# Optimization experiments

Measured on AMD Instinct MI355X. Metric: run time of the kernel, lower is better.

Reference implementation:

```python
import jax, jax.numpy as jnp
import numpy as np

MAX_DISP = 4
RANGE = 2 * MAX_DISP + 1  # 9 -> 80 output channels (center skipped)


def setup_inputs() -> dict:
    key = jax.random.key(0)
    k1, k2 = jax.random.split(key)
    B, C, H, W = 8, 128, 160, 160
    feat1 = jax.random.normal(k1, (B, C, H, W), dtype=jnp.float32)
    feat2 = jax.random.normal(k2, (B, C, H, W), dtype=jnp.float32)
    return {"feat1": feat1, "feat2": feat2}


def cost_volume(feat1, feat2):
    B, C, H, W = feat1.shape
    pad = MAX_DISP
    # zero-pad feat2 spatially by max_displacement on all sides
    feat2_padded = jnp.pad(feat2, ((0, 0), (0, 0), (pad, pad), (pad, pad)))
    vols = []
    for i in range(RANGE):
        for j in range(RANGE):
            if i == pad and j == pad:
                continue  # original skips the zero-displacement center
            feat2_slice = feat2_padded[:, :, i:i + H, j:j + W]  # [B,C,H,W]
            # channel-mean of elementwise product -> [B,1,H,W]
            corr = jnp.mean(feat1 * feat2_slice, axis=1, keepdims=True)
            vols.append(corr)
    return jnp.concatenate(vols, axis=1)  # [B, 80, H, W]


def reference(feat1, feat2):
    return cost_volume(feat1, feat2)
```

## Files before the change

kernel.cpp:

```cpp
#include <hip/hip_runtime.h>

#define BB 8
#define CC_ALL 128
#define HH 160
#define WW 160
#define PAD 4
#define RANGE 9
#define ND 80
#define NG 3
#define DR 3
#define TH 8
#define NTX 40
#define PXT 4
#define NTHREADS 960
#define CCHUNK 8
#define NROWS (TH + DR - 1)
#define ROWF (WW + 2 * PAD)
#define PLANE (HH * WW)
#define NQUADS (CCHUNK * NROWS * (WW / 4))
#define NSLOT 4
#define NACC (RANGE * PXT)

__global__ __launch_bounds__(NTHREADS, 1)
void cost_volume_kernel(const float* __restrict__ f1,
                        const float* __restrict__ f2,
                        float* __restrict__ out) {
    __shared__ __align__(16) float s2[CCHUNK][NROWS][ROWF];

    const int tile_y = blockIdx.x;
    const int bz     = blockIdx.y;
    const int b = bz / NG;
    const int g = bz - b * NG;
    const int h0 = tile_y * TH;
    const int tid = threadIdx.x;
    const int tx = tid % NTX;
    const int r  = (tid / NTX) % DR;
    const int ty = tid / (NTX * DR);
    const int w = tx * PXT;
    const int h = h0 + ty;
    const int row_start = h0 + DR * g - PAD;

    {
        float* p = &s2[0][0][0];
        for (int i = tid; i < CCHUNK * NROWS * ROWF; i += NTHREADS) p[i] = 0.f;
    }

    int glb_off[NSLOT];
    int lds_off[NSLOT];
    unsigned vmask = 0;
    {
#pragma unroll
        for (int k = 0; k < NSLOT; k++) {
            const int s = tid + k * NTHREADS;
            const int quad = s % (WW / 4);
            const int t = s / (WW / 4);
            const int row = t % NROWS;
            const int cc = t / NROWS;
            const int gh = row_start + row;
            glb_off[k] = cc * PLANE + gh * WW + quad * 4;
            lds_off[k] = (cc * NROWS + row) * ROWF + PAD + quad * 4;
            if (s < NQUADS && (unsigned)gh < HH) vmask |= (1u << k);
        }
    }

    float acc[NACC];
#pragma unroll
    for (int i = 0; i < NACC; i++) acc[i] = 0.f;

    const float* f1p = f1 + (size_t)b * CC_ALL * PLANE + (size_t)h * WW + w;
    const float* f2b = f2 + (size_t)b * CC_ALL * PLANE;
    float* s2f = &s2[0][0][0];

    __syncthreads();

    for (int c0 = 0; c0 < CC_ALL; c0 += CCHUNK) {
#pragma unroll
        for (int k = 0; k < NSLOT; k++) {
            if (vmask & (1u << k)) {
                const float4 v = *(const float4*)(f2b + (size_t)c0 * PLANE + glb_off[k]);
                *(float4*)(s2f + lds_off[k]) = v;
            }
        }
        __syncthreads();

#pragma unroll
        for (int cc = 0; cc < CCHUNK; cc++) {
            const float4 a = *(const float4*)(f1p + (size_t)(c0 + cc) * PLANE);
            const float av[PXT] = {a.x, a.y, a.z, a.w};
            const float* rp = &s2[cc][ty + r][w];
            float win[12];
            *(float4*)&win[0] = *(const float4*)(rp);
            *(float4*)&win[4] = *(const float4*)(rp + 4);
            *(float4*)&win[8] = *(const float4*)(rp + 8);
#pragma unroll
            for (int dj = 0; dj < RANGE; dj++) {
#pragma unroll
                for (int p = 0; p < PXT; p++) {
                    acc[dj * PXT + p] += av[p] * win[dj + p];
                }
            }
        }
        __syncthreads();
    }

    float* ob = out + (size_t)b * ND * PLANE + (size_t)h * WW + w;
#pragma unroll
    for (int dj = 0; dj < RANGE; dj++) {
        const int lin = (DR * g + r) * RANGE + dj;
        if (lin == 40) continue;
        const int d = lin - (lin > 40 ? 1 : 0);
        float4 o;
        o.x = acc[dj * PXT + 0] * (1.f / 128.f);
        o.y = acc[dj * PXT + 1] * (1.f / 128.f);
        o.z = acc[dj * PXT + 2] * (1.f / 128.f);
        o.w = acc[dj * PXT + 3] * (1.f / 128.f);
        *(float4*)(ob + (size_t)d * PLANE) = o;
    }
}

extern "C" void kernel_launch(void* const* d_in, const int* in_sizes, int n_in,
                              void* d_out, int out_size, void* d_ws, size_t ws_size,
                              hipStream_t stream) {
    const float* feat1 = (const float*)d_in[0];
    const float* feat2 = (const float*)d_in[1];
    float* out = (float*)d_out;

    dim3 grid(HH / TH, BB * NG);
    dim3 block(NTHREADS);
    cost_volume_kernel<<<grid, block, 0, stream>>>(feat1, feat2, out);
}
```

Before: 346.2 us.

## Double-buffer feat2 LDS tiles with register prefetch to overlap loads and compute

Splits the shared-memory staging of feat2 into two buffers of half the channel chunk. The next chunk is prefetched into registers and written to the alternate buffer while the current one is consumed, which removes one barrier per iteration. The goal is to hide global-load latency behind the FMA work. The cost is more iterations and barriers per channel pass, plus extra registers for the prefetch buffer.

```diff
diff --git a/kernel.cpp b/kernel.cpp
--- a/kernel.cpp
+++ b/kernel.cpp
@@ -13,19 +13,21 @@
 #define NTX 40
 #define PXT 4
 #define NTHREADS 960
-#define CCHUNK 8
+#define CCHUNK 4
+#define NBUF 2
 #define NROWS (TH + DR - 1)
 #define ROWF (WW + 2 * PAD)
+#define BUFF (CCHUNK * NROWS * ROWF)
 #define PLANE (HH * WW)
 #define NQUADS (CCHUNK * NROWS * (WW / 4))
-#define NSLOT 4
+#define NSLOT 2
 #define NACC (RANGE * PXT)
 
 __global__ __launch_bounds__(NTHREADS, 1)
 void cost_volume_kernel(const float* __restrict__ f1,
                         const float* __restrict__ f2,
                         float* __restrict__ out) {
-    __shared__ __align__(16) float s2[CCHUNK][NROWS][ROWF];
+    __shared__ __align__(16) float s2[NBUF][CCHUNK][NROWS][ROWF];
 
     const int tile_y = blockIdx.x;
     const int bz     = blockIdx.y;
@@ -41,8 +43,8 @@
     const int row_start = h0 + DR * g - PAD;
 
     {
-        float* p = &s2[0][0][0];
-        for (int i = tid; i < CCHUNK * NROWS * ROWF; i += NTHREADS) p[i] = 0.f;
+        float* p = &s2[0][0][0][0];
+        for (int i = tid; i < NBUF * BUFF; i += NTHREADS) p[i] = 0.f;
     }
 
     int glb_off[NSLOT];
@@ -69,25 +71,45 @@
 
     const float* f1p = f1 + (size_t)b * CC_ALL * PLANE + (size_t)h * WW + w;
     const float* f2b = f2 + (size_t)b * CC_ALL * PLANE;
-    float* s2f = &s2[0][0][0];
+    float* s2f = &s2[0][0][0][0];
 
+    float4 rbuf[NSLOT];
+#pragma unroll
+    for (int k = 0; k < NSLOT; k++)
+        if (vmask & (1u << k)) rbuf[k] = *(const float4*)(f2b + glb_off[k]);
     __syncthreads();
+#pragma unroll
+    for (int k = 0; k < NSLOT; k++)
+        if (vmask & (1u << k)) *(float4*)(s2f + lds_off[k]) = rbuf[k];
+#pragma unroll
+    for (int k = 0; k < NSLOT; k++)
+        if (vmask & (1u << k))
+            rbuf[k] = *(const float4*)(f2b + (size_t)CCHUNK * PLANE + glb_off[k]);
 
-    for (int c0 = 0; c0 < CC_ALL; c0 += CCHUNK) {
-#pragma unroll
-        for (int k = 0; k < NSLOT; k++) {
-            if (vmask & (1u << k)) {
-                const float4 v = *(const float4*)(f2b + (size_t)c0 * PLANE + glb_off[k]);
-                *(float4*)(s2f + lds_off[k]) = v;
-            }
-        }
+    for (int it = 0; it < CC_ALL / CCHUNK; ++it) {
+        const int c0 = it * CCHUNK;
         __syncthreads();
 
+        const int nbuf_base = ((it + 1) & 1) * BUFF;
+        if (c0 + CCHUNK < CC_ALL) {
+#pragma unroll
+            for (int k = 0; k < NSLOT; k++)
+                if (vmask & (1u << k))
+                    *(float4*)(s2f + nbuf_base + lds_off[k]) = rbuf[k];
+        }
+        if (c0 + 2 * CCHUNK < CC_ALL) {
+#pragma unroll
+            for (int k = 0; k < NSLOT; k++)
+                if (vmask & (1u << k))
+                    rbuf[k] = *(const float4*)(f2b + (size_t)(c0 + 2 * CCHUNK) * PLANE + glb_off[k]);
+        }
+
+        const float* bufp = s2f + (it & 1) * BUFF;
 #pragma unroll
         for (int cc = 0; cc < CCHUNK; cc++) {
             const float4 a = *(const float4*)(f1p + (size_t)(c0 + cc) * PLANE);
             const float av[PXT] = {a.x, a.y, a.z, a.w};
-            const float* rp = &s2[cc][ty + r][w];
+            const float* rp = bufp + (cc * NROWS + ty + r) * ROWF + w;
             float win[12];
             *(float4*)&win[0] = *(const float4*)(rp);
             *(float4*)&win[4] = *(const float4*)(rp + 4);
@@ -100,7 +122,6 @@
                 }
             }
         }
-        __syncthreads();
     }
 
     float* ob = out + (size_t)b * ND * PLANE + (size_t)h * WW + w;
```

Measured after the change: 477.2 us. +37.8%, slower.

## Double-buffer feat2 tiles in LDS using direct global-to-LDS async loads

Applied to the files above, without the earlier changes.

Replaces the register-staged feat2 copy into shared memory with `__builtin_amdgcn_global_load_lds`. Loads go straight into a two-buffer LDS ring with half the channel chunk, so the next chunk is prefetched while the current one is computed. Padding columns and out-of-range rows are filled by loading from a global zero array, which removes the upfront LDS zeroing pass. The cost is doubled LDS footprint, extra zero-source loads, and a reliance on barriers for async-load completion.

```diff
diff --git a/kernel.cpp b/kernel.cpp
--- a/kernel.cpp
+++ b/kernel.cpp
@@ -13,19 +13,30 @@
 #define NTX 40
 #define PXT 4
 #define NTHREADS 960
-#define CCHUNK 8
+#define CCHUNK 4
+#define NBUF 2
 #define NROWS (TH + DR - 1)
 #define ROWF (WW + 2 * PAD)
+#define QROW (ROWF / 4)
+#define NQUADS (CCHUNK * NROWS * QROW)
+#define BSTRIDE (1728 * 4)
 #define PLANE (HH * WW)
-#define NQUADS (CCHUNK * NROWS * (WW / 4))
-#define NSLOT 4
+#define NSLOT 2
 #define NACC (RANGE * PXT)
+#define NCHUNK (CC_ALL / CCHUNK)
+
+__device__ __attribute__((aligned(16))) float g_zero[1024];
+
+#define GLOAD_LDS16(gp, lp)                                                    \
+    __builtin_amdgcn_global_load_lds(                                          \
+        (const __attribute__((address_space(1))) unsigned int*)(gp),           \
+        (__attribute__((address_space(3))) unsigned int*)(lp), 16, 0, 0)
 
 __global__ __launch_bounds__(NTHREADS, 1)
 void cost_volume_kernel(const float* __restrict__ f1,
                         const float* __restrict__ f2,
                         float* __restrict__ out) {
-    __shared__ __align__(16) float s2[CCHUNK][NROWS][ROWF];
+    __shared__ __align__(16) float s2[NBUF * BSTRIDE];
 
     const int tile_y = blockIdx.x;
     const int bz     = blockIdx.y;
@@ -39,28 +50,28 @@
     const int w = tx * PXT;
     const int h = h0 + ty;
     const int row_start = h0 + DR * g - PAD;
+    const int wv = __builtin_amdgcn_readfirstlane(tid >> 6);
 
-    {
-        float* p = &s2[0][0][0];
-        for (int i = tid; i < CCHUNK * NROWS * ROWF; i += NTHREADS) p[i] = 0.f;
-    }
+    const float* f2b = f2 + (size_t)b * CC_ALL * PLANE;
 
-    int glb_off[NSLOT];
-    int lds_off[NSLOT];
-    unsigned vmask = 0;
-    {
+    const float* gsrc[NSLOT];
+    int gstep[NSLOT];
+    bool gval[NSLOT];
+    int lbase[NSLOT];
 #pragma unroll
-        for (int k = 0; k < NSLOT; k++) {
-            const int s = tid + k * NTHREADS;
-            const int quad = s % (WW / 4);
-            const int t = s / (WW / 4);
-            const int row = t % NROWS;
-            const int cc = t / NROWS;
-            const int gh = row_start + row;
-            glb_off[k] = cc * PLANE + gh * WW + quad * 4;
-            lds_off[k] = (cc * NROWS + row) * ROWF + PAD + quad * 4;
-            if (s < NQUADS && (unsigned)gh < HH) vmask |= (1u << k);
-        }
+    for (int k = 0; k < NSLOT; k++) {
+        const int s = tid + k * NTHREADS;
+        const int quad = s % QROW;
+        const int t = s / QROW;
+        const int row = t % NROWS;
+        const int cc = t / NROWS;
+        const int gh = row_start + row;
+        const bool data = (quad >= 1) && (quad <= 40) && ((unsigned)gh < HH);
+        gval[k]  = (s < NQUADS);
+        gsrc[k]  = data ? (f2b + (size_t)cc * PLANE + (size_t)gh * WW + (quad - 1) * 4)
+                        : (g_zero + ((s & 63) << 2));
+        gstep[k] = data ? CCHUNK * PLANE : 0;
+        lbase[k] = (wv * 64 + k * NTHREADS) * 4;
     }
 
     float acc[NACC];
@@ -68,26 +79,35 @@
     for (int i = 0; i < NACC; i++) acc[i] = 0.f;
 
     const float* f1p = f1 + (size_t)b * CC_ALL * PLANE + (size_t)h * WW + w;
-    const float* f2b = f2 + (size_t)b * CC_ALL * PLANE;
-    float* s2f = &s2[0][0][0];
 
+#pragma unroll
+    for (int k = 0; k < NSLOT; k++) {
+        if (gval[k]) {
+            GLOAD_LDS16(gsrc[k], s2 + lbase[k]);
+            gsrc[k] += gstep[k];
+        }
+    }
     __syncthreads();
 
-    for (int c0 = 0; c0 < CC_ALL; c0 += CCHUNK) {
+    for (int it = 0; it < NCHUNK; ++it) {
+        if (it + 1 < NCHUNK) {
+            float* nb = s2 + ((it + 1) & 1) * BSTRIDE;
 #pragma unroll
-        for (int k = 0; k < NSLOT; k++) {
-            if (vmask & (1u << k)) {
-                const float4 v = *(const float4*)(f2b + (size_t)c0 * PLANE + glb_off[k]);
-                *(float4*)(s2f + lds_off[k]) = v;
+            for (int k = 0; k < NSLOT; k++) {
+                if (gval[k]) {
+                    GLOAD_LDS16(gsrc[k], nb + lbase[k]);
+                    gsrc[k] += gstep[k];
+                }
             }
         }
-        __syncthreads();
 
+        const int c0 = it * CCHUNK;
+        const float* bufp = s2 + (it & 1) * BSTRIDE;
 #pragma unroll
         for (int cc = 0; cc < CCHUNK; cc++) {
             const float4 a = *(const float4*)(f1p + (size_t)(c0 + cc) * PLANE);
             const float av[PXT] = {a.x, a.y, a.z, a.w};
-            const float* rp = &s2[cc][ty + r][w];
+            const float* rp = bufp + (cc * NROWS + ty + r) * ROWF + w;
             float win[12];
             *(float4*)&win[0] = *(const float4*)(rp);
             *(float4*)&win[4] = *(const float4*)(rp + 4);
```

Result: faster. 304.8 us (-12.0%).
